# Kernel tuning notes

Hardware: AMD Instinct MI355X
Metric: run time of the kernel (lower is better)

## Reference

```python
import jax, jax.numpy as jnp
import numpy as np

OBS_DIM, ACT_DIM = 512, 32
H1, H2 = 1024, 1024
BATCH = 4096
LOG2PI = float(np.log(2.0 * np.pi))


def setup_inputs() -> dict:
    key = jax.random.key(0)
    ks = jax.random.split(key, 9)
    def uinit(k, shape, fan_in):
        b = 1.0 / np.sqrt(fan_in)
        return jax.random.uniform(k, shape, jnp.float32, -b, b)
    return {
        "obs": jax.random.normal(ks[0], (BATCH, OBS_DIM), jnp.float32),
        "act": jax.random.normal(ks[1], (BATCH, ACT_DIM), jnp.float32),
        # stacked per-head weights: [act_dim, in, out]
        "W1": uinit(ks[2], (ACT_DIM, OBS_DIM, H1), OBS_DIM),
        "b1": uinit(ks[3], (ACT_DIM, H1), OBS_DIM),
        "W2": uinit(ks[4], (ACT_DIM, H1, H2), H1),
        "b2": uinit(ks[5], (ACT_DIM, H2), H1),
        "W3": uinit(ks[6], (ACT_DIM, H2), H2),   # out dim 1, squeezed
        "b3": uinit(ks[7], (ACT_DIM,), H2),
        "log_std": jnp.full((ACT_DIM,), -0.5, jnp.float32),
    }


def reference(obs, act, W1, b1, W2, b2, W3, b3, log_std):
    # act_dim decoupled 3-layer MLPs as batched GEMMs over the head axis 'a'
    x = jnp.tanh(jnp.einsum('bo,aoh->bah', obs, W1) + b1)          # [B, A, H1]
    x = jnp.tanh(jnp.einsum('bah,ahk->bak', x, W2) + b2)           # [B, A, H2]
    mu = jnp.einsum('bak,ak->ba', x, W3) + b3                      # [B, A]
    # diagonal Normal log_prob(act).sum(-1)
    z = (act - mu) * jnp.exp(-log_std)
    logp = jnp.sum(-0.5 * (z * z + LOG2PI) - log_std, axis=-1)     # [B]
    return (mu, logp)
```

## Files before the change

### kernel.cpp

```cpp
#include <hip/hip_runtime.h>
#include <hip/hip_bf16.h>

typedef unsigned short u16;
typedef __bf16 bf16x8 __attribute__((ext_vector_type(8)));
typedef float f32x4 __attribute__((ext_vector_type(4)));

#define LOG2PI_F 1.8378770664093453f

__device__ __forceinline__ u16 f2bf(float f) {
  union { __hip_bfloat16 h; u16 u; } cvt;
  cvt.h = __float2bfloat16(f);
  return cvt.u;
}

__device__ __forceinline__ float fast_tanh(float x) {
  float e = __expf(2.0f * x);
  return 1.0f - 2.0f * __builtin_amdgcn_rcpf(e + 1.0f);
}

__device__ __forceinline__ void load_lds16(const void* g, void* l) {
  __builtin_amdgcn_global_load_lds(
      (const __attribute__((address_space(1))) void*)g,
      (__attribute__((address_space(3))) void*)l,
      16, 0, 0);
}

__global__ void cvt_f32_bf16(const float* __restrict__ in, u16* __restrict__ out, int n4) {
  int i = blockIdx.x * blockDim.x + threadIdx.x;
  int stride = gridDim.x * blockDim.x;
  for (int j = i; j < n4; j += stride) {
    float4 v = reinterpret_cast<const float4*>(in)[j];
    ushort4 o;
    o.x = f2bf(v.x); o.y = f2bf(v.y); o.z = f2bf(v.z); o.w = f2bf(v.w);
    reinterpret_cast<ushort4*>(out)[j] = o;
  }
}

__global__ void transpose_cvt(const float* __restrict__ W, u16* __restrict__ Wt,
                              int K, int N) {
  __shared__ u16 t[64][66];
  const int a = blockIdx.z;
  const int n0 = blockIdx.x * 64, k0 = blockIdx.y * 64;
  const float* Wh = W + (size_t)a * K * N;
  u16* Wth = Wt + (size_t)a * N * K;
  const int tid = threadIdx.x;
#pragma unroll
  for (int j = 0; j < 16; ++j) {
    int idx = j * 256 + tid;
    int r = idx >> 6, c = idx & 63;
    t[r][c] = f2bf(Wh[(size_t)(k0 + r) * N + n0 + c]);
  }
  __syncthreads();
#pragma unroll
  for (int j = 0; j < 16; ++j) {
    int idx = j * 256 + tid;
    int r = idx >> 6, c = idx & 63;
    Wth[(size_t)(n0 + r) * K + k0 + c] = t[c][r];
  }
}

template <int MODE>
__global__ __launch_bounds__(512, 2) void gemm256(
    const u16* __restrict__ A, long aHeadStride,
    const u16* __restrict__ Bt,
    const float* __restrict__ bias,
    int M, int N, int K, int gridN,
    u16* __restrict__ outBf,
    const float* __restrict__ W3,
    float* __restrict__ muAcc) {
  __shared__ __align__(16) u16 lds[2][2][256 * 64];

  const int tid = threadIdx.x;
  const int w = tid >> 6, l = tid & 63;
  const int wm = w >> 2, wn = w & 3;
  const int lh = l & 15, lg = l >> 4;

  const int nwg = gridDim.x;
  const int cpx = nwg >> 3;
  int bid = (blockIdx.x & 7) * cpx + (blockIdx.x >> 3);
  const int bph = (M >> 8) * gridN;
  const int head = bid / bph;
  const int rem = bid % bph;
  const int m0 = (rem / gridN) << 8;
  const int n0 = (rem % gridN) << 8;

  const u16* Ah = A + (size_t)head * (size_t)aHeadStride;
  const u16* Bh = Bt + (size_t)head * (size_t)N * (size_t)K;

  auto stage = [&](int buf, int kt) {
#pragma unroll
    for (int i = 0; i < 4; ++i) {
      int c = i * 512 + tid;
      int row = c >> 3, j = c & 7;
      int js = j ^ (row & 7);
      load_lds16(Ah + (size_t)(m0 + row) * K + kt + js * 8, &lds[buf][0][c * 8]);
    }
#pragma unroll
    for (int i = 0; i < 4; ++i) {
      int c = i * 512 + tid;
      int row = c >> 3, j = c & 7;
      int js = j ^ (row & 7);
      load_lds16(Bh + (size_t)(n0 + row) * K + kt + js * 8, &lds[buf][1][c * 8]);
    }
  };

  f32x4 acc[8][4] = {};
  const int NT = K >> 6;

  stage(0, 0);
  stage(1, 64);
  asm volatile("s_waitcnt vmcnt(8)" ::: "memory");
  __builtin_amdgcn_sched_barrier(0);
  __builtin_amdgcn_s_barrier();

  for (int t = 0; t < NT; ++t) {
    const u16* As = lds[t & 1][0];
    const u16* Bs = lds[t & 1][1];

#pragma unroll
    for (int ks = 0; ks < 2; ++ks) {
      bf16x8 bfr[4];
#pragma unroll
      for (int nf = 0; nf < 4; ++nf) {
        int row = wn * 64 + nf * 16 + lh;
        int j = (ks * 4 + lg) ^ (lh & 7);
        bfr[nf] = *reinterpret_cast<const bf16x8*>(&Bs[row * 64 + j * 8]);
      }
#pragma unroll
      for (int mfh = 0; mfh < 2; ++mfh) {
        bf16x8 af[4];
#pragma unroll
        for (int mi = 0; mi < 4; ++mi) {
          int row = wm * 128 + (mfh * 4 + mi) * 16 + lh;
          int j = (ks * 4 + lg) ^ (lh & 7);
          af[mi] = *reinterpret_cast<const bf16x8*>(&As[row * 64 + j * 8]);
        }
        __builtin_amdgcn_s_setprio(1);
#pragma unroll
        for (int mi = 0; mi < 4; ++mi)
#pragma unroll
          for (int nf = 0; nf < 4; ++nf)
            acc[mfh * 4 + mi][nf] = __builtin_amdgcn_mfma_f32_16x16x32_bf16(
                af[mi], bfr[nf], acc[mfh * 4 + mi][nf], 0, 0, 0);
        __builtin_amdgcn_s_setprio(0);
        __builtin_amdgcn_s_barrier();
      }
    }

    __builtin_amdgcn_sched_barrier(0);
    if (t + 2 < NT) {
      stage(t & 1, (t + 2) << 6);
      asm volatile("s_waitcnt vmcnt(8)" ::: "memory");
    } else {
      asm volatile("s_waitcnt vmcnt(0)" ::: "memory");
    }
    __builtin_amdgcn_sched_barrier(0);
    __builtin_amdgcn_s_barrier();
  }

  if (MODE == 1) {
    u16* Oh = outBf + (size_t)head * (size_t)M * (size_t)N;
#pragma unroll
    for (int mf = 0; mf < 8; ++mf) {
#pragma unroll
      for (int ri = 0; ri < 4; ++ri) {
        const int rowg = m0 + wm * 128 + mf * 16 + lg * 4 + ri;
#pragma unroll
        for (int nf = 0; nf < 4; ++nf) {
          const int col = n0 + wn * 64 + nf * 16 + lh;
          float v = acc[mf][nf][ri] + bias[head * N + col];
          Oh[(size_t)rowg * N + col] = f2bf(fast_tanh(v));
        }
      }
    }
  } else {
#pragma unroll
    for (int mf = 0; mf < 8; ++mf) {
#pragma unroll
      for (int ri = 0; ri < 4; ++ri) {
        const int rowg = m0 + wm * 128 + mf * 16 + lg * 4 + ri;
        float p = 0.f;
#pragma unroll
        for (int nf = 0; nf < 4; ++nf) {
          const int col = n0 + wn * 64 + nf * 16 + lh;
          float v = acc[mf][nf][ri] + bias[head * N + col];
          p += fast_tanh(v) * W3[head * N + col];
        }
        p += __shfl_xor(p, 1);
        p += __shfl_xor(p, 2);
        p += __shfl_xor(p, 4);
        p += __shfl_xor(p, 8);
        if (lh == 0) atomicAdd(&muAcc[(size_t)rowg * 32 + head], p);
      }
    }
  }
}

__global__ void finalize_kernel(const float* __restrict__ muAcc,
                                const float* __restrict__ b3,
                                const float* __restrict__ lstd,
                                const float* __restrict__ act,
                                float* __restrict__ out, int M) {
  int b = blockIdx.x * 256 + threadIdx.x;
  if (b >= M) return;
  float lp = 0.f;
#pragma unroll
  for (int a = 0; a < 32; ++a) {
    float mu = muAcc[(size_t)b * 32 + a] + b3[a];
    out[(size_t)b * 32 + a] = mu;
    float ls = lstd[a];
    float z = (act[(size_t)b * 32 + a] - mu) * __expf(-ls);
    lp += -0.5f * (z * z + LOG2PI_F) - ls;
  }
  out[(size_t)M * 32 + b] = lp;
}

extern "C" void kernel_launch(void* const* d_in, const int* in_sizes, int n_in,
                              void* d_out, int out_size, void* d_ws, size_t ws_size,
                              hipStream_t stream) {
  const float* obs = (const float*)d_in[0];
  const float* act = (const float*)d_in[1];
  const float* W1 = (const float*)d_in[2];
  const float* b1 = (const float*)d_in[3];
  const float* W2 = (const float*)d_in[4];
  const float* b2 = (const float*)d_in[5];
  const float* W3 = (const float*)d_in[6];
  const float* b3 = (const float*)d_in[7];
  const float* lstd = (const float*)d_in[8];

  constexpr int B = 4096, OBS = 512, A = 32, H1 = 1024, H2 = 1024;

  u16* obs_bf = (u16*)d_ws;
  u16* W1t = obs_bf + (size_t)B * OBS;
  u16* W2t = W1t + (size_t)A * H1 * OBS;
  u16* x1 = W2t + (size_t)A * H2 * H1;
  float* muAcc = (float*)(x1 + (size_t)A * B * H1);
  float* out = (float*)d_out;

  hipMemsetAsync(muAcc, 0, (size_t)B * A * sizeof(float), stream);

  cvt_f32_bf16<<<1024, 256, 0, stream>>>(obs, obs_bf, B * OBS / 4);
  transpose_cvt<<<dim3(H1 / 64, OBS / 64, A), 256, 0, stream>>>(W1, W1t, OBS, H1);
  transpose_cvt<<<dim3(H2 / 64, H1 / 64, A), 256, 0, stream>>>(W2, W2t, H1, H2);

  gemm256<1><<<(B / 256) * (H1 / 256) * A, 512, 0, stream>>>(
      obs_bf, 0L, W1t, b1, B, H1, OBS, H1 / 256, x1, nullptr, nullptr);

  gemm256<2><<<(B / 256) * (H2 / 256) * A, 512, 0, stream>>>(
      x1, (long)B * H1, W2t, b2, B, H2, H1, H2 / 256, nullptr, W3, muAcc);

  finalize_kernel<<<B / 256, 256, 0, stream>>>(muAcc, b3, lstd, act, out, B);
}
```

Before: 813.1 us.

## Interleave half-tile global-to-LDS prefetches with MFMA phases in 8-phase ping-pong loop

Restructures the GEMM main loop into an unrolled two-tile, eight-phase schedule. Each phase loads B fragments for a whole k-tile once and A fragments for a 32-row slice, then issues 16 MFMAs. The next tiles' half-size global-to-LDS loads are spread across these phases instead of issued all at once after the compute, so memory traffic overlaps compute more evenly. It adds many more workgroup barriers and finer vmcnt accounting, which could stall the waves or create LDS hazards if the counts are off.

```diff
diff --git a/kernel.cpp b/kernel.cpp
--- a/kernel.cpp
+++ b/kernel.cpp
@@ -60,7 +60,7 @@
 }
 
 template <int MODE>
-__global__ __launch_bounds__(512, 2) void gemm256(
+__global__ __launch_bounds__(512, 2) void gemm256p(
     const u16* __restrict__ A, long aHeadStride,
     const u16* __restrict__ Bt,
     const float* __restrict__ bias,
@@ -75,9 +75,8 @@
   const int wm = w >> 2, wn = w & 3;
   const int lh = l & 15, lg = l >> 4;
 
-  const int nwg = gridDim.x;
-  const int cpx = nwg >> 3;
-  int bid = (blockIdx.x & 7) * cpx + (blockIdx.x >> 3);
+  const int cpx = gridDim.x >> 3;
+  const int bid = (blockIdx.x & 7) * cpx + (blockIdx.x >> 3);
   const int bph = (M >> 8) * gridN;
   const int head = bid / bph;
   const int rem = bid % bph;
@@ -87,89 +86,159 @@
   const u16* Ah = A + (size_t)head * (size_t)aHeadStride;
   const u16* Bh = Bt + (size_t)head * (size_t)N * (size_t)K;
 
-  auto stage = [&](int buf, int kt) {
-#pragma unroll
-    for (int i = 0; i < 4; ++i) {
-      int c = i * 512 + tid;
+  auto stageH = [&](int T, int op, int h) {
+    const u16* src = (op == 0) ? Ah : Bh;
+    const int base = (op == 0) ? m0 : n0;
+    const int kt = T << 6;
+    u16* dst = &lds[T & 1][op][h * (128 * 64)];
+#pragma unroll
+    for (int s = 0; s < 2; ++s) {
+      int c = s * 512 + tid;
       int row = c >> 3, j = c & 7;
       int js = j ^ (row & 7);
-      load_lds16(Ah + (size_t)(m0 + row) * K + kt + js * 8, &lds[buf][0][c * 8]);
-    }
-#pragma unroll
-    for (int i = 0; i < 4; ++i) {
-      int c = i * 512 + tid;
-      int row = c >> 3, j = c & 7;
-      int js = j ^ (row & 7);
-      load_lds16(Bh + (size_t)(n0 + row) * K + kt + js * 8, &lds[buf][1][c * 8]);
+      load_lds16(src + (size_t)(base + h * 128 + row) * K + kt + js * 8,
+                 dst + c * 8);
     }
   };
 
   f32x4 acc[8][4] = {};
+  bf16x8 bq[4][2];
+  const u16* const As0 = lds[0][0];
+  const u16* const Bs0 = lds[0][1];
+  const u16* const As1 = lds[1][0];
+  const u16* const Bs1 = lds[1][1];
   const int NT = K >> 6;
 
-  stage(0, 0);
-  stage(1, 64);
-  asm volatile("s_waitcnt vmcnt(8)" ::: "memory");
+#define LDB(Bs)                                                              \
+  _Pragma("unroll")                                                          \
+  for (int nf = 0; nf < 4; ++nf)                                             \
+    _Pragma("unroll")                                                        \
+    for (int ks = 0; ks < 2; ++ks) {                                         \
+      const int row = wn * 64 + nf * 16 + lh;                                \
+      const int j = (ks * 4 + lg) ^ (lh & 7);                                \
+      bq[nf][ks] = *reinterpret_cast<const bf16x8*>(&(Bs)[row * 64 + j * 8]); \
+    }
+
+#define LDA(As, P, af)                                                       \
+  _Pragma("unroll")                                                          \
+  for (int q = 0; q < 2; ++q)                                                \
+    _Pragma("unroll")                                                        \
+    for (int ks = 0; ks < 2; ++ks) {                                         \
+      const int row = wm * 128 + (2 * (P) + q) * 16 + lh;                    \
+      const int j = (ks * 4 + lg) ^ (lh & 7);                                \
+      af[q][ks] = *reinterpret_cast<const bf16x8*>(&(As)[row * 64 + j * 8]); \
+    }
+
+#define MFMA16(P, af)                                                        \
+  __builtin_amdgcn_s_setprio(1);                                             \
+  _Pragma("unroll")                                                          \
+  for (int ks = 0; ks < 2; ++ks)                                             \
+    _Pragma("unroll")                                                        \
+    for (int q = 0; q < 2; ++q)                                              \
+      _Pragma("unroll")                                                      \
+      for (int nf = 0; nf < 4; ++nf)                                         \
+        acc[2 * (P) + q][nf] = __builtin_amdgcn_mfma_f32_16x16x32_bf16(      \
+            af[q][ks], bq[nf][ks], acc[2 * (P) + q][nf], 0, 0, 0);           \
+  __builtin_amdgcn_s_setprio(0);
+
+  stageH(0, 1, 0); stageH(0, 1, 1);
+  stageH(0, 0, 0); stageH(0, 0, 1);
+  stageH(1, 1, 0); stageH(1, 1, 1);
+  asm volatile("s_waitcnt vmcnt(4)" ::: "memory");
   __builtin_amdgcn_sched_barrier(0);
   __builtin_amdgcn_s_barrier();
 
-  for (int t = 0; t < NT; ++t) {
-    const u16* As = lds[t & 1][0];
-    const u16* Bs = lds[t & 1][1];
-
-#pragma unroll
-    for (int ks = 0; ks < 2; ++ks) {
-      bf16x8 bfr[4];
-#pragma unroll
-      for (int nf = 0; nf < 4; ++nf) {
-        int row = wn * 64 + nf * 16 + lh;
-        int j = (ks * 4 + lg) ^ (lh & 7);
-        bfr[nf] = *reinterpret_cast<const bf16x8*>(&Bs[row * 64 + j * 8]);
+  for (int i = 0; i < NT / 2; ++i) {
+    const int t0 = 2 * i;
+    const bool pref = (t0 + 2) < NT;
+
+    {
+      bf16x8 af[2][2];
+      LDB(Bs0);
+      LDA(As0, 0, af);
+      __builtin_amdgcn_s_barrier();
+      MFMA16(0, af);
+      __builtin_amdgcn_s_barrier();
+    }
+    {
+      bf16x8 af[2][2];
+      LDA(As0, 1, af);
+      stageH(t0 + 1, 0, 0); stageH(t0 + 1, 0, 1);
+      __builtin_amdgcn_s_barrier();
+      MFMA16(1, af);
+      __builtin_amdgcn_s_barrier();
+    }
+    {
+      bf16x8 af[2][2];
+      LDA(As0, 2, af);
+      if (pref) { stageH(t0 + 2, 1, 0); stageH(t0 + 2, 1, 1); }
+      __builtin_amdgcn_s_barrier();
+      MFMA16(2, af);
+      __builtin_amdgcn_s_barrier();
+    }
+    {
+      bf16x8 af[2][2];
+      LDA(As0, 3, af);
+      __builtin_amdgcn_s_barrier();
+      MFMA16(3, af);
+      if (pref) asm volatile("s_waitcnt vmcnt(4)" ::: "memory");
+      else      asm volatile("s_waitcnt vmcnt(0)" ::: "memory");
+      __builtin_amdgcn_sched_barrier(0);
+      __builtin_amdgcn_s_barrier();
+    }
+    {
+      bf16x8 af[2][2];
+      LDB(Bs1);
+      LDA(As1, 0, af);
+      if (pref) { stageH(t0 + 2, 0, 0); stageH(t0 + 2, 0, 1); }
+      __builtin_amdgcn_s_barrier();
+      MFMA16(0, af);
+      __builtin_amdgcn_s_barrier();
+    }
+    {
+      bf16x8 af[2][2];
+      LDA(As1, 1, af);
+      if (pref) { stageH(t0 + 3, 1, 0); stageH(t0 + 3, 1, 1); }
+      __builtin_amdgcn_s_barrier();
+      MFMA16(1, af);
+      __builtin_amdgcn_s_barrier();
+    }
+    {
+      bf16x8 af[2][2];
+      LDA(As1, 2, af);
+      __builtin_amdgcn_s_barrier();
+      MFMA16(2, af);
+      __builtin_amdgcn_s_barrier();
+    }
+    {
+      bf16x8 af[2][2];
+      LDA(As1, 3, af);
+      __builtin_amdgcn_s_barrier();
+      MFMA16(3, af);
+      if (pref) {
+        asm volatile("s_waitcnt vmcnt(4)" ::: "memory");
+        __builtin_amdgcn_sched_barrier(0);
       }
-#pragma unroll
-      for (int mfh = 0; mfh < 2; ++mfh) {
-        bf16x8 af[4];
-#pragma unroll
-        for (int mi = 0; mi < 4; ++mi) {
-          int row = wm * 128 + (mfh * 4 + mi) * 16 + lh;
-          int j = (ks * 4 + lg) ^ (lh & 7);
-          af[mi] = *reinterpret_cast<const bf16x8*>(&As[row * 64 + j * 8]);
-        }
-        __builtin_amdgcn_s_setprio(1);
-#pragma unroll
-        for (int mi = 0; mi < 4; ++mi)
-#pragma unroll
-          for (int nf = 0; nf < 4; ++nf)
-            acc[mfh * 4 + mi][nf] = __builtin_amdgcn_mfma_f32_16x16x32_bf16(
-                af[mi], bfr[nf], acc[mfh * 4 + mi][nf], 0, 0, 0);
-        __builtin_amdgcn_s_setprio(0);
-        __builtin_amdgcn_s_barrier();
-      }
-    }
-
-    __builtin_amdgcn_sched_barrier(0);
-    if (t + 2 < NT) {
-      stage(t & 1, (t + 2) << 6);
-      asm volatile("s_waitcnt vmcnt(8)" ::: "memory");
-    } else {
-      asm volatile("s_waitcnt vmcnt(0)" ::: "memory");
-    }
-    __builtin_amdgcn_sched_barrier(0);
-    __builtin_amdgcn_s_barrier();
-  }
+      __builtin_amdgcn_s_barrier();
+    }
+  }
+
+#undef LDB
+#undef LDA
+#undef MFMA16
 
   if (MODE == 1) {
     u16* Oh = outBf + (size_t)head * (size_t)M * (size_t)N;
 #pragma unroll
     for (int mf = 0; mf < 8; ++mf) {
 #pragma unroll
-      for (int ri = 0; ri < 4; ++ri) {
-        const int rowg = m0 + wm * 128 + mf * 16 + lg * 4 + ri;
+      for (int r = 0; r < 4; ++r) {
+        const int row = m0 + wm * 128 + mf * 16 + lg * 4 + r;
 #pragma unroll
         for (int nf = 0; nf < 4; ++nf) {
           const int col = n0 + wn * 64 + nf * 16 + lh;
-          float v = acc[mf][nf][ri] + bias[head * N + col];
-          Oh[(size_t)rowg * N + col] = f2bf(fast_tanh(v));
+          float v = acc[mf][nf][r] + bias[head * N + col];
+          Oh[(size_t)row * N + col] = f2bf(fast_tanh(v));
         }
       }
     }
@@ -177,20 +246,20 @@
 #pragma unroll
     for (int mf = 0; mf < 8; ++mf) {
 #pragma unroll
-      for (int ri = 0; ri < 4; ++ri) {
-        const int rowg = m0 + wm * 128 + mf * 16 + lg * 4 + ri;
+      for (int r = 0; r < 4; ++r) {
+        const int row = m0 + wm * 128 + mf * 16 + lg * 4 + r;
         float p = 0.f;
 #pragma unroll
         for (int nf = 0; nf < 4; ++nf) {
           const int col = n0 + wn * 64 + nf * 16 + lh;
-          float v = acc[mf][nf][ri] + bias[head * N + col];
+          float v = acc[mf][nf][r] + bias[head * N + col];
           p += fast_tanh(v) * W3[head * N + col];
         }
         p += __shfl_xor(p, 1);
         p += __shfl_xor(p, 2);
         p += __shfl_xor(p, 4);
         p += __shfl_xor(p, 8);
-        if (lh == 0) atomicAdd(&muAcc[(size_t)rowg * 32 + head], p);
+        if (lh == 0) atomicAdd(&muAcc[(size_t)row * 32 + head], p);
       }
     }
   }
@@ -243,10 +312,10 @@
   transpose_cvt<<<dim3(H1 / 64, OBS / 64, A), 256, 0, stream>>>(W1, W1t, OBS, H1);
   transpose_cvt<<<dim3(H2 / 64, H1 / 64, A), 256, 0, stream>>>(W2, W2t, H1, H2);
 
-  gemm256<1><<<(B / 256) * (H1 / 256) * A, 512, 0, stream>>>(
+  gemm256p<1><<<(B / 256) * (H1 / 256) * A, 512, 0, stream>>>(
       obs_bf, 0L, W1t, b1, B, H1, OBS, H1 / 256, x1, nullptr, nullptr);
 
-  gemm256<2><<<(B / 256) * (H2 / 256) * A, 512, 0, stream>>>(
+  gemm256p<2><<<(B / 256) * (H2 / 256) * A, 512, 0, stream>>>(
       x1, (long)B * H1, W2t, b2, B, H2, H1, H2 / 256, nullptr, W3, muAcc);
 
   finalize_kernel<<<B / 256, 256, 0, stream>>>(muAcc, b3, lstd, act, out, B);
```

New measurement: 770.1 us. 5.3% less time.
